# Kernel optimization log

Measured on AMD Instinct MI355X. Metric: run time of the kernel, lower is better.

Reference implementation:

```python
import jax, jax.numpy as jnp
from jax import lax
import numpy as np

DECAY = 0.9
THRESH = 1.0


def setup_inputs() -> dict:
    key = jax.random.key(0)
    k1, k2, k3 = jax.random.split(key, 3)
    B, T, I, H, O = 64, 256, 1024, 2048, 1024
    x = jax.random.normal(k1, (B, T, I), dtype=jnp.float32)
    W1 = jax.random.normal(k2, (I, H), dtype=jnp.float32) * (1.0 / np.sqrt(I))
    b1 = jnp.zeros((H,), dtype=jnp.float32)
    W2 = jax.random.normal(k3, (H, O), dtype=jnp.float32) * (1.0 / np.sqrt(H))
    b2 = jnp.zeros((O,), dtype=jnp.float32)
    return {"x": x, "W1": W1, "b1": b1, "W2": W2, "b2": b2}


def reference(x, W1, b1, W2, b2):
    B, T, I = x.shape
    H = W1.shape[1]
    # Batch fc1 across all timesteps in one GEMM: [B,T,H]
    cur = jnp.einsum('bti,ih->bth', x, W1) + b1
    cur_tm = jnp.swapaxes(cur, 0, 1)  # [T,B,H] time-major for scan

    def step(carry, cur_t):
        mem, _ = carry
        mem = mem * DECAY + cur_t * (1.0 - DECAY)
        fired = mem > THRESH
        spk = jnp.where(fired, 1.0, 0.0).astype(mem.dtype)
        mem = jnp.where(fired, 0.0, mem)
        return (mem, spk), None

    mem0 = jnp.zeros((B, H), dtype=x.dtype)
    spk0 = jnp.zeros((B, H), dtype=x.dtype)
    (_, spk_last), _ = lax.scan(step, (mem0, spk0), cur_tm)
    # fc2 applied only to the final spike pattern, as in the original
    return spk_last @ W2 + b2
```

## Files before the change

kernel.cpp:

```cpp
#include <hip/hip_runtime.h>


typedef __attribute__((ext_vector_type(16))) float f32x16;
typedef __attribute__((ext_vector_type(8))) short s16x8;

#define GPTR(p) ((const __attribute__((address_space(1))) void*)(p))
#define SPTR(p) ((__attribute__((address_space(3))) void*)(p))

static constexpr int Bsz = 64, Tsz = 256, Isz = 1024, Hsz = 2048, Osz = 1024;
static constexpr int BK = 32;
static constexpr int NKT = Isz / BK;
static constexpr int AH_OFF = 0, AL_OFF = 8192, BH_OFF = 16384, BL_OFF = 24576;
static constexpr int BUFEL = 32768;
static constexpr int ST = 132;
static constexpr int LDS_USHORTS = 256 * ST * 2;

__device__ __forceinline__ unsigned short f2bf(float f) {
  unsigned u = __float_as_uint(f);
  u += 0x7FFFu + ((u >> 16) & 1u);
  return (unsigned short)(u >> 16);
}
__device__ __forceinline__ float bf2f(unsigned short h) {
  return __uint_as_float(((unsigned)h) << 16);
}

__global__ void split_x_kernel(const float* __restrict__ x,
                               unsigned short* __restrict__ hi,
                               unsigned short* __restrict__ lo) {
  const long i = (long)blockIdx.x * 256 + threadIdx.x;
  const float4 v = ((const float4*)x)[i];
  const unsigned short hx = f2bf(v.x), hy = f2bf(v.y), hz = f2bf(v.z), hw = f2bf(v.w);
  ushort4 H, L;
  H.x = hx; H.y = hy; H.z = hz; H.w = hw;
  L.x = f2bf(v.x - bf2f(hx));
  L.y = f2bf(v.y - bf2f(hy));
  L.z = f2bf(v.z - bf2f(hz));
  L.w = f2bf(v.w - bf2f(hw));
  ((ushort4*)hi)[i] = H;
  ((ushort4*)lo)[i] = L;
}

__global__ void w1_transpose_split_kernel(const float* __restrict__ W1,
                                          unsigned short* __restrict__ wh,
                                          unsigned short* __restrict__ wl) {
  __shared__ float tile[32][33];
  const int h0 = blockIdx.x * 32;
  const int i0 = blockIdx.y * 32;
  const int c = threadIdx.x & 31;
  const int r4 = threadIdx.x >> 5;
#pragma unroll
  for (int s = 0; s < 4; ++s) {
    const int r = r4 + s * 8;
    tile[r][c] = W1[(long)(i0 + r) * Hsz + h0 + c];
  }
  __syncthreads();
#pragma unroll
  for (int s = 0; s < 4; ++s) {
    const int hr = r4 + s * 8;
    const float v = tile[c][hr];
    const unsigned short hh = f2bf(v);
    wh[(long)(h0 + hr) * Isz + i0 + c] = hh;
    wl[(long)(h0 + hr) * Isz + i0 + c] = f2bf(v - bf2f(hh));
  }
}

__global__ __launch_bounds__(256, 1) void gemm1_scan_kernel(
    const unsigned short* __restrict__ xh, const unsigned short* __restrict__ xl,
    const unsigned short* __restrict__ wth, const unsigned short* __restrict__ wtl,
    const float* __restrict__ b1, float* __restrict__ spk) {
  __shared__ __align__(16) unsigned short lds[LDS_USHORTS];

  const int tid = threadIdx.x;
  const int l = tid & 63;
  const int w = tid >> 6;
  const int wm = w >> 1;
  const int wn = w & 1;
  const int b = blockIdx.y;
  const int hb = blockIdx.x * 256;

  const int srow = tid >> 2;
  const int gch8 = ((tid & 3) ^ ((tid >> 3) & 3)) * 8;
  const unsigned short* gAh = xh + (long)(b * Tsz + srow) * Isz + gch8;
  const unsigned short* gAl = xl + (long)(b * Tsz + srow) * Isz + gch8;
  const unsigned short* gBh = wth + (long)(hb + srow) * Isz + gch8;
  const unsigned short* gBl = wtl + (long)(hb + srow) * Isz + gch8;

#define STG(OFF, G, KT) do {                                                              \
    unsigned short* d_ = lds + ((KT) & 1) * BUFEL + (OFF) + tid * 8;                      \
    __builtin_amdgcn_global_load_lds(GPTR((G) + (long)(KT) * BK), SPTR(d_), 16, 0, 0);    \
    __builtin_amdgcn_global_load_lds(GPTR((G) + 64 * Isz + (long)(KT) * BK), SPTR(d_ + 2048), 16, 0, 0); \
    __builtin_amdgcn_global_load_lds(GPTR((G) + 128 * Isz + (long)(KT) * BK), SPTR(d_ + 4096), 16, 0, 0); \
    __builtin_amdgcn_global_load_lds(GPTR((G) + 192 * Isz + (long)(KT) * BK), SPTR(d_ + 6144), 16, 0, 0); \
  } while (0)

  const int lr = l & 31;
  const int swzf = (l >> 1) & 3;
  const int chK0 = (((l >> 5)) ^ swzf) * 8;
  const int chK1 = ((2 + (l >> 5)) ^ swzf) * 8;
  const int abase = (wm * 128 + lr) * 32;
  const int bbase = (wn * 128 + lr) * 32;

  f32x16 acc[4][4];
#pragma unroll
  for (int i = 0; i < 4; ++i)
#pragma unroll
    for (int j = 0; j < 4; ++j) acc[i][j] = (f32x16)(0.f);

#define MM(MI, NI, AF, BF) \
  acc[MI][NI] = __builtin_amdgcn_mfma_f32_32x32x16_bf16(AF, BF, acc[MI][NI], 0, 0, 0)

#define BAR() __builtin_amdgcn_s_barrier()
#define SBAR() __builtin_amdgcn_sched_barrier(0)
#define WAITLGKM(N) do { asm volatile("s_waitcnt lgkmcnt(" #N ")" ::: "memory"); SBAR(); } while (0)

  STG(AH_OFF, gAh, 0);
  STG(BH_OFF, gBh, 0);
  STG(AL_OFF, gAl, 0);
  STG(BL_OFF, gBl, 0);
  asm volatile("s_waitcnt vmcnt(0)" ::: "memory");
  BAR();

  s16x8 Ah0[4], Ah1[4], Al0[4], Al1[4], Bh0[4], Bh1[4], Bl0[4], Bl1[4];

  for (int kt = 0; kt < NKT; ++kt) {
    const unsigned short* p = lds + (kt & 1) * BUFEL;
    const bool st = (kt + 1) < NKT;

#pragma unroll
    for (int mi = 0; mi < 4; ++mi) Ah0[mi] = *(const s16x8*)(p + AH_OFF + abase + mi * 1024 + chK0);
#pragma unroll
    for (int ni = 0; ni < 4; ++ni) Bh0[ni] = *(const s16x8*)(p + BH_OFF + bbase + ni * 1024 + chK0);
    SBAR();
#pragma unroll
    for (int mi = 0; mi < 4; ++mi) Ah1[mi] = *(const s16x8*)(p + AH_OFF + abase + mi * 1024 + chK1);
#pragma unroll
    for (int ni = 0; ni < 4; ++ni) Bh1[ni] = *(const s16x8*)(p + BH_OFF + bbase + ni * 1024 + chK1);
    SBAR();
    if (st) { STG(AH_OFF, gAh, kt + 1); STG(BH_OFF, gBh, kt + 1);
              STG(AL_OFF, gAl, kt + 1); STG(BL_OFF, gBl, kt + 1); }
    SBAR();
    WAITLGKM(8);
    __builtin_amdgcn_s_setprio(1);
#pragma unroll
    for (int mi = 0; mi < 4; ++mi)
#pragma unroll
      for (int ni = 0; ni < 4; ++ni) MM(mi, ni, Ah0[mi], Bh0[ni]);
    SBAR();
#pragma unroll
    for (int ni = 0; ni < 4; ++ni) {
      Bl0[ni] = *(const s16x8*)(p + BL_OFF + bbase + ni * 1024 + chK0);
      Bl1[ni] = *(const s16x8*)(p + BL_OFF + bbase + ni * 1024 + chK1);
    }
    WAITLGKM(8);
#pragma unroll
    for (int mi = 0; mi < 4; ++mi)
#pragma unroll
      for (int ni = 0; ni < 4; ++ni) MM(mi, ni, Ah1[mi], Bh1[ni]);
    SBAR();
#pragma unroll
    for (int mi = 0; mi < 4; ++mi) {
      Al0[mi] = *(const s16x8*)(p + AL_OFF + abase + mi * 1024 + chK0);
      Al1[mi] = *(const s16x8*)(p + AL_OFF + abase + mi * 1024 + chK1);
    }
    WAITLGKM(8);
#pragma unroll
    for (int mi = 0; mi < 4; ++mi)
#pragma unroll
      for (int ni = 0; ni < 4; ++ni) MM(mi, ni, Ah0[mi], Bl0[ni]);
#pragma unroll
    for (int mi = 0; mi < 4; ++mi)
#pragma unroll
      for (int ni = 0; ni < 4; ++ni) MM(mi, ni, Ah1[mi], Bl1[ni]);
    WAITLGKM(0);
#pragma unroll
    for (int mi = 0; mi < 4; ++mi)
#pragma unroll
      for (int ni = 0; ni < 4; ++ni) MM(mi, ni, Al0[mi], Bh0[ni]);
#pragma unroll
    for (int mi = 0; mi < 4; ++mi)
#pragma unroll
      for (int ni = 0; ni < 4; ++ni) MM(mi, ni, Al1[mi], Bh1[ni]);
    __builtin_amdgcn_s_setprio(0);
    asm volatile("s_waitcnt vmcnt(0)" ::: "memory");
    BAR();
  }

  __syncthreads();
  float* scanbuf = reinterpret_cast<float*>(lds);
  float memv = 0.f;
  int fired = 0;
  const float b1v = b1[hb + tid];

  for (int rnd = 0; rnd < 2; ++rnd) {
    if (wm == rnd) {
#pragma unroll
      for (int mi = 0; mi < 4; ++mi)
#pragma unroll
        for (int ni = 0; ni < 4; ++ni) {
          const int col = wn * 128 + ni * 32 + lr;
          float* dst = scanbuf + col * ST + mi * 32 + 4 * (l >> 5);
#pragma unroll
          for (int rq = 0; rq < 4; ++rq) {
            float4 v;
            v.x = acc[mi][ni][rq * 4 + 0];
            v.y = acc[mi][ni][rq * 4 + 1];
            v.z = acc[mi][ni][rq * 4 + 2];
            v.w = acc[mi][ni][rq * 4 + 3];
            *reinterpret_cast<float4*>(dst + 8 * rq) = v;
          }
        }
    }
    __syncthreads();
    {
      const float* src = scanbuf + tid * ST;
      float4 cur = *reinterpret_cast<const float4*>(src);
      for (int t0 = 0; t0 < 128; t0 += 4) {
        const int tn = (t0 + 4 < 128) ? t0 + 4 : t0;
        const float4 nxt = *reinterpret_cast<const float4*>(src + tn);
        float c;
        c = cur.x + b1v; memv = memv * 0.9f + c * 0.1f; fired = memv > 1.0f; if (fired) memv = 0.f;
        c = cur.y + b1v; memv = memv * 0.9f + c * 0.1f; fired = memv > 1.0f; if (fired) memv = 0.f;
        c = cur.z + b1v; memv = memv * 0.9f + c * 0.1f; fired = memv > 1.0f; if (fired) memv = 0.f;
        c = cur.w + b1v; memv = memv * 0.9f + c * 0.1f; fired = memv > 1.0f; if (fired) memv = 0.f;
        cur = nxt;
      }
    }
    __syncthreads();
  }
  spk[(long)b * Hsz + hb + tid] = fired ? 1.0f : 0.0f;
}

__global__ void gemm2_kernel(const float* __restrict__ spk, const float* __restrict__ W2,
                             const float* __restrict__ b2, float* __restrict__ out) {
  __shared__ int s_cnt[256];
  __shared__ int s_off[257];
  __shared__ int s_list[Hsz];
  const int b = blockIdx.x;
  const int tid = threadIdx.x;
  int hs[8];
  int c = 0;
#pragma unroll
  for (int e = 0; e < 8; ++e) {
    const int h = tid * 8 + e;
    if (spk[(long)b * Hsz + h] > 0.5f) hs[c++] = h;
  }
  s_cnt[tid] = c;
  __syncthreads();
  if (tid == 0) {
    int s = 0;
    for (int i = 0; i < 256; ++i) { s_off[i] = s; s += s_cnt[i]; }
    s_off[256] = s;
  }
  __syncthreads();
  {
    const int base = s_off[tid];
    for (int i = 0; i < c; ++i) s_list[base + i] = hs[i];
  }
  __syncthreads();
  const int total = s_off[256];
#pragma unroll
  for (int q = 0; q < 4; ++q) {
    const int o = q * 256 + tid;
    float v = b2[o];
    for (int i = 0; i < total; ++i) v += W2[(long)s_list[i] * Osz + o];
    out[(long)b * Osz + o] = v;
  }
}

extern "C" void kernel_launch(void* const* d_in, const int* in_sizes, int n_in,
                              void* d_out, int out_size, void* d_ws, size_t ws_size,
                              hipStream_t stream) {
  const float* x = (const float*)d_in[0];
  const float* W1 = (const float*)d_in[1];
  const float* b1 = (const float*)d_in[2];
  const float* W2 = (const float*)d_in[3];
  const float* b2 = (const float*)d_in[4];
  float* out = (float*)d_out;

  unsigned short* xh = (unsigned short*)d_ws;
  unsigned short* xl = xh + (long)Bsz * Tsz * Isz;
  unsigned short* wh = xl + (long)Bsz * Tsz * Isz;
  unsigned short* wl = wh + (long)Hsz * Isz;
  float* spk = (float*)(wl + (long)Hsz * Isz);

  split_x_kernel<<<(Bsz * Tsz * Isz) / (256 * 4), 256, 0, stream>>>(x, xh, xl);
  w1_transpose_split_kernel<<<dim3(Hsz / 32, Isz / 32), 256, 0, stream>>>(W1, wh, wl);
  gemm1_scan_kernel<<<dim3(8, 64), 256, 0, stream>>>(xh, xl, wh, wl, b1, spk);
  gemm2_kernel<<<Bsz, 256, 0, stream>>>(spk, W2, b2, out);
}
```

Baseline: 210.5 us.

## Use 512-thread blocks, BK=16, and triple-buffered LDS pipeline in gemm1

Restructures the fused GEMM+scan kernel to use 8 waves per block, each computing a 128x64 tile, and shrinks the K step to 16. LDS becomes a three-stage ring buffer with prefetch two iterations ahead, and the LDS swizzle is removed. Launch bounds now allow two blocks per CU to raise occupancy and hide latency. The scan is split into four rounds of 64 timesteps, with only half the threads doing scan work. Risks include more barriers per K, bank conflicts from the unswizzled layout, and idle threads during the scan.

```diff
diff --git a/kernel.cpp b/kernel.cpp
--- a/kernel.cpp
+++ b/kernel.cpp
@@ -8,12 +8,13 @@
 #define SPTR(p) ((__attribute__((address_space(3))) void*)(p))
 
 static constexpr int Bsz = 64, Tsz = 256, Isz = 1024, Hsz = 2048, Osz = 1024;
-static constexpr int BK = 32;
+static constexpr int BK = 16;
 static constexpr int NKT = Isz / BK;
-static constexpr int AH_OFF = 0, AL_OFF = 8192, BH_OFF = 16384, BL_OFF = 24576;
-static constexpr int BUFEL = 32768;
-static constexpr int ST = 132;
-static constexpr int LDS_USHORTS = 256 * ST * 2;
+static constexpr int REG = 4096;
+static constexpr int AH_OFF = 0, AL_OFF = REG, BH_OFF = 2 * REG, BL_OFF = 3 * REG;
+static constexpr int BUFEL = 4 * REG;
+static constexpr int ST = 68;
+static constexpr int LDS_USHORTS = 3 * BUFEL;
 
 __device__ __forceinline__ unsigned short f2bf(float f) {
   unsigned u = __float_as_uint(f);
@@ -64,7 +65,7 @@
   }
 }
 
-__global__ __launch_bounds__(256, 1) void gemm1_scan_kernel(
+__global__ __launch_bounds__(512, 2) void gemm1_scan_kernel(
     const unsigned short* __restrict__ xh, const unsigned short* __restrict__ xl,
     const unsigned short* __restrict__ wth, const unsigned short* __restrict__ wtl,
     const float* __restrict__ b1, float* __restrict__ spk) {
@@ -73,38 +74,32 @@
   const int tid = threadIdx.x;
   const int l = tid & 63;
   const int w = tid >> 6;
-  const int wm = w >> 1;
-  const int wn = w & 1;
+  const int wm = w >> 2;
+  const int wn = w & 3;
   const int b = blockIdx.y;
   const int hb = blockIdx.x * 256;
 
-  const int srow = tid >> 2;
-  const int gch8 = ((tid & 3) ^ ((tid >> 3) & 3)) * 8;
+  const int srow = tid >> 1;
+  const int gch8 = (tid & 1) * 8;
   const unsigned short* gAh = xh + (long)(b * Tsz + srow) * Isz + gch8;
   const unsigned short* gAl = xl + (long)(b * Tsz + srow) * Isz + gch8;
   const unsigned short* gBh = wth + (long)(hb + srow) * Isz + gch8;
   const unsigned short* gBl = wtl + (long)(hb + srow) * Isz + gch8;
 
-#define STG(OFF, G, KT) do {                                                              \
-    unsigned short* d_ = lds + ((KT) & 1) * BUFEL + (OFF) + tid * 8;                      \
+#define STG(OFF, G, Q, KT) do {                                                           \
+    unsigned short* d_ = lds + (Q) * BUFEL + (OFF) + tid * 8;                             \
     __builtin_amdgcn_global_load_lds(GPTR((G) + (long)(KT) * BK), SPTR(d_), 16, 0, 0);    \
-    __builtin_amdgcn_global_load_lds(GPTR((G) + 64 * Isz + (long)(KT) * BK), SPTR(d_ + 2048), 16, 0, 0); \
-    __builtin_amdgcn_global_load_lds(GPTR((G) + 128 * Isz + (long)(KT) * BK), SPTR(d_ + 4096), 16, 0, 0); \
-    __builtin_amdgcn_global_load_lds(GPTR((G) + 192 * Isz + (long)(KT) * BK), SPTR(d_ + 6144), 16, 0, 0); \
   } while (0)
 
   const int lr = l & 31;
-  const int swzf = (l >> 1) & 3;
-  const int chK0 = (((l >> 5)) ^ swzf) * 8;
-  const int chK1 = ((2 + (l >> 5)) ^ swzf) * 8;
-  const int abase = (wm * 128 + lr) * 32;
-  const int bbase = (wn * 128 + lr) * 32;
-
-  f32x16 acc[4][4];
+  const int abase = (wm * 128 + lr) * BK + (l >> 5) * 8;
+  const int bbase = (wn * 64 + lr) * BK + (l >> 5) * 8;
+
+  f32x16 acc[4][2];
 #pragma unroll
   for (int i = 0; i < 4; ++i)
 #pragma unroll
-    for (int j = 0; j < 4; ++j) acc[i][j] = (f32x16)(0.f);
+    for (int j = 0; j < 2; ++j) acc[i][j] = (f32x16)(0.f);
 
 #define MM(MI, NI, AF, BF) \
   acc[MI][NI] = __builtin_amdgcn_mfma_f32_32x32x16_bf16(AF, BF, acc[MI][NI], 0, 0, 0)
@@ -113,92 +108,72 @@
 #define SBAR() __builtin_amdgcn_sched_barrier(0)
 #define WAITLGKM(N) do { asm volatile("s_waitcnt lgkmcnt(" #N ")" ::: "memory"); SBAR(); } while (0)
 
-  STG(AH_OFF, gAh, 0);
-  STG(BH_OFF, gBh, 0);
-  STG(AL_OFF, gAl, 0);
-  STG(BL_OFF, gBl, 0);
-  asm volatile("s_waitcnt vmcnt(0)" ::: "memory");
+  STG(AH_OFF, gAh, 0, 0); STG(AL_OFF, gAl, 0, 0);
+  STG(BH_OFF, gBh, 0, 0); STG(BL_OFF, gBl, 0, 0);
+  STG(AH_OFF, gAh, 1, 1); STG(AL_OFF, gAl, 1, 1);
+  STG(BH_OFF, gBh, 1, 1); STG(BL_OFF, gBl, 1, 1);
+  asm volatile("s_waitcnt vmcnt(4)" ::: "memory");
   BAR();
 
-  s16x8 Ah0[4], Ah1[4], Al0[4], Al1[4], Bh0[4], Bh1[4], Bl0[4], Bl1[4];
-
+  s16x8 Ah[4], Al[4], Bh[2], Bl[2];
+
+  int q = 0;
   for (int kt = 0; kt < NKT; ++kt) {
-    const unsigned short* p = lds + (kt & 1) * BUFEL;
-    const bool st = (kt + 1) < NKT;
-
-#pragma unroll
-    for (int mi = 0; mi < 4; ++mi) Ah0[mi] = *(const s16x8*)(p + AH_OFF + abase + mi * 1024 + chK0);
-#pragma unroll
-    for (int ni = 0; ni < 4; ++ni) Bh0[ni] = *(const s16x8*)(p + BH_OFF + bbase + ni * 1024 + chK0);
+    const unsigned short* p = lds + q * BUFEL;
+    const int qn = (q >= 1) ? q - 1 : 2;
+    const bool st = (kt + 2) < NKT;
+
+#pragma unroll
+    for (int mi = 0; mi < 4; ++mi) Ah[mi] = *(const s16x8*)(p + AH_OFF + abase + mi * 512);
+#pragma unroll
+    for (int ni = 0; ni < 2; ++ni) Bh[ni] = *(const s16x8*)(p + BH_OFF + bbase + ni * 512);
     SBAR();
 #pragma unroll
-    for (int mi = 0; mi < 4; ++mi) Ah1[mi] = *(const s16x8*)(p + AH_OFF + abase + mi * 1024 + chK1);
-#pragma unroll
-    for (int ni = 0; ni < 4; ++ni) Bh1[ni] = *(const s16x8*)(p + BH_OFF + bbase + ni * 1024 + chK1);
+    for (int mi = 0; mi < 4; ++mi) Al[mi] = *(const s16x8*)(p + AL_OFF + abase + mi * 512);
+#pragma unroll
+    for (int ni = 0; ni < 2; ++ni) Bl[ni] = *(const s16x8*)(p + BL_OFF + bbase + ni * 512);
     SBAR();
-    if (st) { STG(AH_OFF, gAh, kt + 1); STG(BH_OFF, gBh, kt + 1);
-              STG(AL_OFF, gAl, kt + 1); STG(BL_OFF, gBl, kt + 1); }
+    if (st) { STG(AH_OFF, gAh, qn, kt + 2); STG(AL_OFF, gAl, qn, kt + 2);
+              STG(BH_OFF, gBh, qn, kt + 2); STG(BL_OFF, gBl, qn, kt + 2); }
     SBAR();
-    WAITLGKM(8);
+    WAITLGKM(6);
     __builtin_amdgcn_s_setprio(1);
 #pragma unroll
     for (int mi = 0; mi < 4; ++mi)
 #pragma unroll
-      for (int ni = 0; ni < 4; ++ni) MM(mi, ni, Ah0[mi], Bh0[ni]);
-    SBAR();
-#pragma unroll
-    for (int ni = 0; ni < 4; ++ni) {
-      Bl0[ni] = *(const s16x8*)(p + BL_OFF + bbase + ni * 1024 + chK0);
-      Bl1[ni] = *(const s16x8*)(p + BL_OFF + bbase + ni * 1024 + chK1);
-    }
-    WAITLGKM(8);
+      for (int ni = 0; ni < 2; ++ni) MM(mi, ni, Ah[mi], Bh[ni]);
+    WAITLGKM(0);
 #pragma unroll
     for (int mi = 0; mi < 4; ++mi)
 #pragma unroll
-      for (int ni = 0; ni < 4; ++ni) MM(mi, ni, Ah1[mi], Bh1[ni]);
-    SBAR();
-#pragma unroll
-    for (int mi = 0; mi < 4; ++mi) {
-      Al0[mi] = *(const s16x8*)(p + AL_OFF + abase + mi * 1024 + chK0);
-      Al1[mi] = *(const s16x8*)(p + AL_OFF + abase + mi * 1024 + chK1);
-    }
-    WAITLGKM(8);
+      for (int ni = 0; ni < 2; ++ni) MM(mi, ni, Ah[mi], Bl[ni]);
 #pragma unroll
     for (int mi = 0; mi < 4; ++mi)
 #pragma unroll
-      for (int ni = 0; ni < 4; ++ni) MM(mi, ni, Ah0[mi], Bl0[ni]);
-#pragma unroll
-    for (int mi = 0; mi < 4; ++mi)
-#pragma unroll
-      for (int ni = 0; ni < 4; ++ni) MM(mi, ni, Ah1[mi], Bl1[ni]);
-    WAITLGKM(0);
-#pragma unroll
-    for (int mi = 0; mi < 4; ++mi)
-#pragma unroll
-      for (int ni = 0; ni < 4; ++ni) MM(mi, ni, Al0[mi], Bh0[ni]);
-#pragma unroll
-    for (int mi = 0; mi < 4; ++mi)
-#pragma unroll
-      for (int ni = 0; ni < 4; ++ni) MM(mi, ni, Al1[mi], Bh1[ni]);
+      for (int ni = 0; ni < 2; ++ni) MM(mi, ni, Al[mi], Bh[ni]);
     __builtin_amdgcn_s_setprio(0);
-    asm volatile("s_waitcnt vmcnt(0)" ::: "memory");
+    if (st) asm volatile("s_waitcnt vmcnt(4)" ::: "memory");
+    else    asm volatile("s_waitcnt vmcnt(0)" ::: "memory");
     BAR();
+    q = (q == 2) ? 0 : q + 1;
   }
 
   __syncthreads();
   float* scanbuf = reinterpret_cast<float*>(lds);
   float memv = 0.f;
   int fired = 0;
-  const float b1v = b1[hb + tid];
-
-  for (int rnd = 0; rnd < 2; ++rnd) {
-    if (wm == rnd) {
-#pragma unroll
-      for (int mi = 0; mi < 4; ++mi)
-#pragma unroll
-        for (int ni = 0; ni < 4; ++ni) {
-          const int col = wn * 128 + ni * 32 + lr;
-          float* dst = scanbuf + col * ST + mi * 32 + 4 * (l >> 5);
+  const float b1v = (tid < 256) ? b1[hb + tid] : 0.f;
+
+  for (int rnd = 0; rnd < 4; ++rnd) {
+    if (wm == (rnd >> 1)) {
+      const int mi0 = (rnd & 1) * 2;
+#pragma unroll
+      for (int dm = 0; dm < 2; ++dm) {
+        const int mi = mi0 + dm;
+#pragma unroll
+        for (int ni = 0; ni < 2; ++ni) {
+          const int col = wn * 64 + ni * 32 + lr;
+          float* dst = scanbuf + col * ST + dm * 32 + 4 * (l >> 5);
 #pragma unroll
           for (int rq = 0; rq < 4; ++rq) {
             float4 v;
@@ -209,13 +184,14 @@
             *reinterpret_cast<float4*>(dst + 8 * rq) = v;
           }
         }
+      }
     }
     __syncthreads();
-    {
+    if (tid < 256) {
       const float* src = scanbuf + tid * ST;
       float4 cur = *reinterpret_cast<const float4*>(src);
-      for (int t0 = 0; t0 < 128; t0 += 4) {
-        const int tn = (t0 + 4 < 128) ? t0 + 4 : t0;
+      for (int t0 = 0; t0 < 64; t0 += 4) {
+        const int tn = (t0 + 4 < 64) ? t0 + 4 : t0;
         const float4 nxt = *reinterpret_cast<const float4*>(src + tn);
         float c;
         c = cur.x + b1v; memv = memv * 0.9f + c * 0.1f; fired = memv > 1.0f; if (fired) memv = 0.f;
@@ -227,7 +203,7 @@
     }
     __syncthreads();
   }
-  spk[(long)b * Hsz + hb + tid] = fired ? 1.0f : 0.0f;
+  if (tid < 256) spk[(long)b * Hsz + hb + tid] = fired ? 1.0f : 0.0f;
 }
 
 __global__ void gemm2_kernel(const float* __restrict__ spk, const float* __restrict__ W2,
@@ -285,6 +261,6 @@
 
   split_x_kernel<<<(Bsz * Tsz * Isz) / (256 * 4), 256, 0, stream>>>(x, xh, xl);
   w1_transpose_split_kernel<<<dim3(Hsz / 32, Isz / 32), 256, 0, stream>>>(W1, wh, wl);
-  gemm1_scan_kernel<<<dim3(8, 64), 256, 0, stream>>>(xh, xl, wh, wl, b1, spk);
+  gemm1_scan_kernel<<<dim3(8, 64), 512, 0, stream>>>(xh, xl, wh, wl, b1, spk);
   gemm2_kernel<<<Bsz, 256, 0, stream>>>(spk, W2, b2, out);
 }
```

After: 218.6 us. 3.9% more time.
